# Performance work log

Measured on AMD Instinct MI355X. Metric: run time of the kernel, lower is better.

Reference implementation:

```python
import jax, jax.numpy as jnp
import numpy as np
from jax import lax

WS = 8            # window size
N = WS * WS       # tokens per window = 64
HEADS = 4
QKV_DIM = 16      # per-head dim
INNER = HEADS * QKV_DIM  # 64
SCALE = 1.0 / float(np.sqrt(QKV_DIM))


def setup_inputs() -> dict:
    key = jax.random.key(0)
    ks = jax.random.split(key, 8)
    B, C, H, W = 8, 96, 192, 192
    O = 96
    p = lambda k, shape, s=0.02: jax.random.normal(k, shape, dtype=jnp.float32) * s
    return {
        "x": jax.random.normal(ks[0], (B, C, H, W), dtype=jnp.float32),
        "bias": p(ks[1], (1, N)),                   # learned per-window bias seed
        "bias_proj_w": p(ks[2], (N * N, N)),        # Linear(N, N*N, bias=False)
        "qkv_w": p(ks[3], (3 * INNER, C)),
        "qkv_b": jnp.zeros((3 * INNER,), jnp.float32),
        "out_w": p(ks[4], (C, INNER)),
        "out_b": jnp.zeros((C,), jnp.float32),
        "conv1_w": p(ks[5], (O, C, 1, 1)),
        "conv1_b": jnp.zeros((O,), jnp.float32),
        "conv2_w": p(ks[6], (O, O, 3, 3)),
        "conv2_b": jnp.zeros((O,), jnp.float32),
    }


def _leaky(x):
    return jnp.where(x >= 0, x, 0.1 * x)


def reference(x, bias, bias_proj_w, qkv_w, qkv_b, out_w, out_b,
              conv1_w, conv1_b, conv2_w, conv2_b):
    B, C, H, W = x.shape
    nh, nw = H // WS, W // WS

    # learned attention bias: Linear(N -> N*N) on (1,N) seed, viewed as (N,N)
    attn_bias = (bias @ bias_proj_w.T).reshape(N, N)

    # --- Window MHA (norm1 = Identity) ---
    # window partition: (B, C, H, W) -> (B*nh*nw, N, C)
    xw = x.reshape(B, C, nh, WS, nw, WS).transpose(0, 2, 4, 3, 5, 1)
    xw = xw.reshape(B * nh * nw, N, C)

    qkv = xw @ qkv_w.T + qkv_b                     # (Bw, N, 3*INNER)
    qkv = qkv.reshape(-1, N, 3, HEADS, QKV_DIM)
    q = qkv[:, :, 0].transpose(0, 2, 1, 3)         # (Bw, H, N, d)
    k = qkv[:, :, 1].transpose(0, 2, 1, 3)
    v = qkv[:, :, 2].transpose(0, 2, 1, 3)

    scores = jnp.einsum('bhnd,bhmd->bhnm', q, k) * SCALE + attn_bias
    attn = jax.nn.softmax(scores, axis=-1)
    o = jnp.einsum('bhnm,bhmd->bhnd', attn, v)     # (Bw, H, N, d)
    o = o.transpose(0, 2, 1, 3).reshape(-1, N, INNER)
    o = o @ out_w.T + out_b                        # (Bw, N, C)

    # window merge: (B*nh*nw, N, C) -> (B, C, H, W)
    o = o.reshape(B, nh, nw, WS, WS, C).transpose(0, 5, 1, 3, 2, 4)
    o = o.reshape(B, C, H, W)

    x = x + o                                      # residual

    # --- conv MLP: 1x1 conv -> LeakyReLU(0.1) -> 3x3 conv (replicate pad) -> LeakyReLU(0.1) ---
    h = jnp.einsum('oc,bchw->bohw', conv1_w[:, :, 0, 0], x) + conv1_b[None, :, None, None]
    h = _leaky(h)
    hp = jnp.pad(h, ((0, 0), (0, 0), (1, 1), (1, 1)), mode='edge')
    h = lax.conv_general_dilated(hp, conv2_w, (1, 1), 'VALID',
                                 dimension_numbers=('NCHW', 'OIHW', 'NCHW'))
    h = _leaky(h + conv2_b[None, :, None, None])

    # in_channels == out_channels -> proj is Identity
    return x + h
```

## Files before the change

### kernel.cpp

```cpp
#include <hip/hip_runtime.h>
#include <hip/hip_bf16.h>

typedef __attribute__((ext_vector_type(8))) short short8;
typedef __attribute__((ext_vector_type(4))) short short4v;
typedef __attribute__((ext_vector_type(4))) float floatx4;

#define MFMA16x32(a,b,c) __builtin_amdgcn_mfma_f32_16x16x32_bf16((a),(b),(c),0,0,0)

static __device__ __forceinline__ unsigned short f2b(float f) {
  __hip_bfloat16 h = __float2bfloat16(f);
  return __builtin_bit_cast(unsigned short, h);
}
static __device__ __forceinline__ float b2f(unsigned short u) {
  __hip_bfloat16 h = __builtin_bit_cast(__hip_bfloat16, u);
  return __bfloat162float(h);
}

#define HH 192
#define WWID 192
#define HW (192*192)

#define YX_OFF   0
#define H1_OFF   56623104
#define AB_OFF   113246208
#define QKVW_OFF 113262592
#define OUTW_OFF 113299456
#define W1_OFF   113311744
#define W2R_OFF  113330176

__global__ __launch_bounds__(256) void k_prep(
    const float* __restrict__ bias, const float* __restrict__ bpw,
    const float* __restrict__ qkv_w, const float* __restrict__ out_w,
    const float* __restrict__ w1, const float* __restrict__ w2,
    char* __restrict__ ws) {
  int tid = blockIdx.x * blockDim.x + threadIdx.x;
  int nth = gridDim.x * blockDim.x;
  float* ab = (float*)(ws + AB_OFF);
  unsigned short* qkvw = (unsigned short*)(ws + QKVW_OFF);
  unsigned short* outw = (unsigned short*)(ws + OUTW_OFF);
  unsigned short* w1b  = (unsigned short*)(ws + W1_OFF);
  unsigned short* w2r  = (unsigned short*)(ws + W2R_OFF);

  for (int i = tid; i < 4096; i += nth) {
    float s = 0.f;
    #pragma unroll 8
    for (int k = 0; k < 64; k++) s += bias[k] * bpw[i*64 + k];
    int c = i & 63;
    ab[(i & ~63) + ((c & 15) << 2) + (c >> 4)] = s;
  }
  for (int i = tid; i < 192*96; i += nth) qkvw[i] = f2b(qkv_w[i]);
  for (int i = tid; i < 96*64;  i += nth) outw[i] = f2b(out_w[i]);
  for (int i = tid; i < 96*96;  i += nth) w1b[i]  = f2b(w1[i]);
  for (int i = tid; i < 96*864; i += nth) {
    int o = i / 864, k = i % 864;
    int tap = k / 96, c = k % 96;
    w2r[i] = f2b(w2[(o*96 + c)*9 + tap]);
  }
}

__global__ __launch_bounds__(256) void k_xt(
    const float* __restrict__ x, unsigned short* __restrict__ xt) {
  __shared__ __align__(16) float tile[96*65];
  int blk = blockIdx.x;
  int b = blk / 576, rem = blk % 576;
  int i = rem / 3, j0 = (rem % 3) * 64;
  int tid = threadIdx.x;
  const float* xb = x + (size_t)b*96*HW + (size_t)i*WWID + j0;

  for (int f = tid; f < 1536; f += 256) {
    int c = f >> 4, q = f & 15;
    *(floatx4*)&tile[c*65 + 4*q] = *(const floatx4*)&xb[(size_t)c*HW + 4*q];
  }
  __syncthreads();
  unsigned short* xtb = xt + ((size_t)b*HW + (size_t)i*WWID + j0) * 96;
  for (int f = tid; f < 768; f += 256) {
    int p = f / 12, c0 = (f % 12) * 8;
    short8 o;
    #pragma unroll
    for (int u = 0; u < 8; u++) o[u] = (short)f2b(tile[(c0+u)*65 + p]);
    *(short8*)&xtb[p*96 + c0] = o;
  }
}

__global__ __launch_bounds__(256,4) void k_attn(
    unsigned short* yx, const float* __restrict__ qkv_b,
    const float* __restrict__ out_b, const float* __restrict__ b1,
    const char* __restrict__ wsr, unsigned short* __restrict__ h1) {
  __shared__ __align__(16) char smem[33792];
  unsigned short* vt   = (unsigned short*)smem;
  unsigned short* qkw  = (unsigned short*)(smem + 9216);
  unsigned short* o64  = (unsigned short*)smem;
  unsigned short* ybuf = (unsigned short*)(smem + 9216);

  const float* ab = (const float*)(wsr + AB_OFF);
  const unsigned short* qkvw = (const unsigned short*)(wsr + QKVW_OFF);
  const unsigned short* outw = (const unsigned short*)(wsr + OUTW_OFF);
  const unsigned short* w1b  = (const unsigned short*)(wsr + W1_OFF);

  int blk = blockIdx.x;
  int b = blk / 576, rem = blk % 576;
  int wi = rem / 24, wj = rem % 24;
  int h0 = wi * 8, w0 = wj * 8;
  unsigned short* xtw = yx + (size_t)b*HW*96;
  unsigned short* h1w = h1 + (size_t)b*HW*96;

  int tid = threadIdx.x;
  int h = tid >> 6, ln = tid & 63;
  int row = ln & 15, kg = ln >> 4;

  unsigned short* qh = qkw + h*3072;
  unsigned short* kh = qh + 1536;
  unsigned short* pch = qh;

  const floatx4 zf = {0.f, 0.f, 0.f, 0.f};
  const short8 zs = {0,0,0,0,0,0,0,0};

  floatx4 accq[4][3];
  #pragma unroll
  for (int m = 0; m < 4; m++)
    #pragma unroll
    for (int n = 0; n < 3; n++) accq[m][n] = zf;
  #pragma unroll
  for (int ks = 0; ks < 3; ks++) {
    int c0 = ks*32 + kg*8;
    short8 a[4], bb[3];
    #pragma unroll
    for (int m = 0; m < 4; m++) {
      int t = m*16 + row;
      a[m] = *(const short8*)&xtw[((size_t)((h0 + (t>>3))*WWID + w0 + (t&7)))*96 + c0];
    }
    #pragma unroll
    for (int n = 0; n < 3; n++)
      bb[n] = *(const short8*)&qkvw[((n*4 + h)*16 + row)*96 + c0];
    #pragma unroll
    for (int m = 0; m < 4; m++)
      #pragma unroll
      for (int n = 0; n < 3; n++) accq[m][n] = MFMA16x32(a[m], bb[n], accq[m][n]);
  }
  float qb0 = qkv_b[h*16 + row], qb1 = qkv_b[64 + h*16 + row], qb2 = qkv_b[128 + h*16 + row];
  #pragma unroll
  for (int m = 0; m < 4; m++) {
    #pragma unroll
    for (int r = 0; r < 4; r++) {
      int t = m*16 + kg*4 + r;
      qh[t*24 + row] = f2b(accq[m][0][r] + qb0);
      kh[t*24 + row] = f2b(accq[m][1][r] + qb1);
    }
    short4v vv;
    #pragma unroll
    for (int r = 0; r < 4; r++) vv[r] = (short)f2b(accq[m][2][r] + qb2);
    *(short4v*)&vt[(h*16 + row)*72 + m*16 + kg*4] = vv;
  }
  asm volatile("" ::: "memory");

  short8 kb[4];
  #pragma unroll
  for (int n = 0; n < 4; n++)
    kb[n] = (kg < 2) ? *(const short8*)&kh[(n*16 + row)*24 + kg*8] : zs;
  unsigned pw[4][4][2];
  float inv[4][4];
  #pragma unroll
  for (int m = 0; m < 4; m++) {
    short8 qa = (kg < 2) ? *(const short8*)&qh[(m*16 + row)*24 + kg*8] : zs;
    floatx4 sc[4];
    #pragma unroll
    for (int n = 0; n < 4; n++) sc[n] = MFMA16x32(qa, kb[n], zf);
    #pragma unroll
    for (int r = 0; r < 4; r++) {
      int t = m*16 + kg*4 + r;
      floatx4 abv = *(const floatx4*)&ab[t*64 + row*4];
      float e0 = __expf(sc[0][r]*0.25f + abv[0]);
      float e1 = __expf(sc[1][r]*0.25f + abv[1]);
      float e2 = __expf(sc[2][r]*0.25f + abv[2]);
      float e3 = __expf(sc[3][r]*0.25f + abv[3]);
      float s = (e0 + e1) + (e2 + e3);
      #pragma unroll
      for (int d = 1; d < 16; d <<= 1) s += __shfl_xor(s, d, 64);
      inv[m][r] = 1.0f / s;
      pw[m][r][0] = (unsigned)f2b(e0) | ((unsigned)f2b(e1) << 16);
      pw[m][r][1] = (unsigned)f2b(e2) | ((unsigned)f2b(e3) << 16);
    }
  }

  floatx4 ov[4];
  #pragma unroll
  for (int m = 0; m < 4; m++) ov[m] = zf;
  #pragma unroll
  for (int ksk = 0; ksk < 2; ksk++) {
    asm volatile("" ::: "memory");
    #pragma unroll
    for (int m = 0; m < 4; m++)
      #pragma unroll
      for (int r = 0; r < 4; r++) {
        int t = m*16 + kg*4 + r;
        unsigned w = pw[m][r][ksk];
        pch[t*40 + row]      = (unsigned short)w;
        pch[t*40 + 16 + row] = (unsigned short)(w >> 16);
      }
    asm volatile("" ::: "memory");
    short8 vb = *(const short8*)&vt[(h*16 + row)*72 + ksk*32 + kg*8];
    #pragma unroll
    for (int m = 0; m < 4; m++) {
      short8 pa = *(const short8*)&pch[(m*16 + row)*40 + kg*8];
      ov[m] = MFMA16x32(pa, vb, ov[m]);
    }
  }
  __syncthreads();

  #pragma unroll
  for (int m = 0; m < 4; m++)
    #pragma unroll
    for (int r = 0; r < 4; r++)
      o64[(m*16 + kg*4 + r)*72 + h*16 + row] = f2b(ov[m][r] * inv[m][r]);
  __syncthreads();

  floatx4 op[6];
  #pragma unroll
  for (int n = 0; n < 6; n++) op[n] = zf;
  #pragma unroll
  for (int ks = 0; ks < 2; ks++) {
    short8 ao = *(const short8*)&o64[(h*16 + row)*72 + ks*32 + kg*8];
    #pragma unroll
    for (int n = 0; n < 6; n++) {
      short8 bo = *(const short8*)&outw[(n*16 + row)*64 + ks*32 + kg*8];
      op[n] = MFMA16x32(ao, bo, op[n]);
    }
  }

  #pragma unroll
  for (int n = 0; n < 6; n++) {
    int o = n*16 + row;
    float ob = out_b[o];
    #pragma unroll
    for (int r = 0; r < 4; r++) {
      int t = h*16 + kg*4 + r;
      int gi = h0 + (t>>3), gj = w0 + (t&7);
      size_t gx = ((size_t)(gi*WWID + gj))*96 + o;
      float yv = op[n][r] + ob + b2f(xtw[gx]);
      unsigned short yb = f2b(yv);
      xtw[gx] = yb;
      ybuf[t*104 + o] = yb;
    }
  }
  asm volatile("" ::: "memory");

  floatx4 ac1[6];
  #pragma unroll
  for (int n = 0; n < 6; n++) ac1[n] = zf;
  #pragma unroll
  for (int ks = 0; ks < 3; ks++) {
    int c0 = ks*32 + kg*8;
    short8 ay = *(const short8*)&ybuf[(h*16 + row)*104 + c0];
    #pragma unroll
    for (int n = 0; n < 6; n++) {
      short8 bw = *(const short8*)&w1b[(n*16 + row)*96 + c0];
      ac1[n] = MFMA16x32(ay, bw, ac1[n]);
    }
  }
  #pragma unroll
  for (int n = 0; n < 6; n++) {
    int o = n*16 + row;
    float bo = b1[o];
    #pragma unroll
    for (int r = 0; r < 4; r++) {
      int t = h*16 + kg*4 + r;
      int gi = h0 + (t>>3), gj = w0 + (t&7);
      float v = ac1[n][r] + bo;
      v = v >= 0.f ? v : 0.1f*v;
      h1w[((size_t)(gi*WWID + gj))*96 + o] = f2b(v);
    }
  }
}

#define C2_CS 2760

__global__ __launch_bounds__(512,4) void k_conv2(
    const unsigned short* __restrict__ h1, const unsigned short* __restrict__ y,
    const float* __restrict__ b2, const char* __restrict__ wsr,
    float* __restrict__ out) {
  __shared__ __align__(16) char smem[66304];
  unsigned short* h1t = (unsigned short*)smem;
  float* ost = (float*)smem;
  const unsigned short* w2r = (const unsigned short*)(wsr + W2R_OFF);
  int blk = blockIdx.x;
  int b = blk / 144, rem = blk % 144;
  int i0 = (rem / 6) * 8, j0 = (rem % 6) * 32;
  int tid = threadIdx.x;

  for (int idx = tid; idx < 4080; idx += 512) {
    int pix = idx / 12, c8 = idx % 12;
    int hr = pix / 34, hc = pix % 34;
    int gi = min(max(i0 + hr - 1, 0), 191);
    int gj = min(max(j0 + hc - 1, 0), 191);
    *(short8*)&h1t[c8*C2_CS + pix*8] =
        *(const short8*)&h1[((size_t)b*HW + (size_t)gi*WWID + gj)*96 + c8*8];
  }
  __syncthreads();

  int wv = tid >> 6, ln = tid & 63;
  int row = ln & 15, kg = ln >> 4;
  int og = wv >> 2, pg = wv & 3;

  const floatx4 zf = {0.f, 0.f, 0.f, 0.f};
  floatx4 acc[3][4];
  #pragma unroll
  for (int m = 0; m < 3; m++)
    #pragma unroll
    for (int n = 0; n < 4; n++) acc[m][n] = zf;

  #pragma unroll
  for (int s = 0; s < 27; s++) {
    int tap = s / 3, di = tap / 3, dj = tap % 3;
    int cq = (s % 3)*4 + kg;
    short8 a[3], bb[4];
    #pragma unroll
    for (int m = 0; m < 3; m++)
      a[m] = *(const short8*)&w2r[(og*48 + m*16 + row)*864 + s*32 + kg*8];
    #pragma unroll
    for (int n = 0; n < 4; n++) {
      int p = pg*64 + n*16 + row;
      int pr = p >> 5, pc = p & 31;
      int pix = (pr + di)*34 + pc + dj;
      bb[n] = *(const short8*)&h1t[cq*C2_CS + pix*8];
    }
    #pragma unroll
    for (int m = 0; m < 3; m++)
      #pragma unroll
      for (int n = 0; n < 4; n++)
        acc[m][n] = MFMA16x32(a[m], bb[n], acc[m][n]);
  }
  __syncthreads();

  #pragma unroll
  for (int pass = 0; pass < 2; pass++) {
    if (og == pass) {
      #pragma unroll
      for (int m = 0; m < 3; m++) {
        #pragma unroll
        for (int r = 0; r < 4; r++) {
          int o2 = m*16 + kg*4 + r;
          int o = og*48 + o2;
          float bo = b2[o];
          #pragma unroll
          for (int n = 0; n < 4; n++) {
            int p = pg*64 + n*16 + row;
            int pr = p >> 5, pc = p & 31;
            float hv = acc[m][n][r] + bo;
            hv = hv >= 0.f ? hv : 0.1f*hv;
            float yv = b2f(y[((size_t)b*HW + (size_t)(i0+pr)*WWID + j0+pc)*96 + o]);
            ost[o2*260 + pr*32 + pc] = yv + hv;
          }
        }
      }
    }
    __syncthreads();
    for (int c = tid; c < 3072; c += 512) {
      int o2 = c >> 6, rq = c & 63;
      int pr = rq >> 3, q = rq & 7;
      floatx4 v = *(const floatx4*)&ost[o2*260 + pr*32 + q*4];
      int o = pass*48 + o2;
      *(floatx4*)&out[((size_t)(b*96 + o)*HH + i0 + pr)*WWID + j0 + q*4] = v;
    }
    __syncthreads();
  }
}

extern "C" void kernel_launch(void* const* d_in, const int* in_sizes, int n_in,
                              void* d_out, int out_size, void* d_ws, size_t ws_size,
                              hipStream_t stream) {
  const float* x    = (const float*)d_in[0];
  const float* bias = (const float*)d_in[1];
  const float* bpw  = (const float*)d_in[2];
  const float* qkvw = (const float*)d_in[3];
  const float* qkvb = (const float*)d_in[4];
  const float* outw = (const float*)d_in[5];
  const float* outb = (const float*)d_in[6];
  const float* w1   = (const float*)d_in[7];
  const float* b1   = (const float*)d_in[8];
  const float* w2   = (const float*)d_in[9];
  const float* b2   = (const float*)d_in[10];

  char* ws = (char*)d_ws;
  float* out = (float*)d_out;
  unsigned short* yx = (unsigned short*)(ws + YX_OFF);
  unsigned short* h1 = (unsigned short*)(ws + H1_OFF);

  k_prep<<<128, 256, 0, stream>>>(bias, bpw, qkvw, outw, w1, w2, ws);
  k_xt  <<<4608, 256, 0, stream>>>(x, yx);
  k_attn<<<4608, 256, 0, stream>>>(yx, qkvb, outb, b1, ws, h1);
  k_conv2<<<1152, 512, 0, stream>>>(h1, yx, b2, ws, out);
}
```

Measured before the change: 267.0 us.

## Switch conv2 LDS tile to pixel-major padded layout and store output directly

Changes the conv2 shared-memory tile from a channel-group-major layout to a pixel-major layout with 104-element padded rows. It also removes the LDS-staged two-pass epilogue, writing results straight to global memory from the accumulators, and drops the full unroll of the 27-step tap loop. This is meant to cut LDS footprint and barriers and to change bank-conflict behaviour on the B-operand reads. In exchange, the output stores become strided scalar writes instead of coalesced float4 rows.

```diff
diff --git a/kernel.cpp b/kernel.cpp
--- a/kernel.cpp
+++ b/kernel.cpp
@@ -272,15 +272,11 @@
   }
 }
 
-#define C2_CS 2760
-
 __global__ __launch_bounds__(512,4) void k_conv2(
     const unsigned short* __restrict__ h1, const unsigned short* __restrict__ y,
     const float* __restrict__ b2, const char* __restrict__ wsr,
     float* __restrict__ out) {
-  __shared__ __align__(16) char smem[66304];
-  unsigned short* h1t = (unsigned short*)smem;
-  float* ost = (float*)smem;
+  __shared__ __align__(16) unsigned short h1t[340*104];
   const unsigned short* w2r = (const unsigned short*)(wsr + W2R_OFF);
   int blk = blockIdx.x;
   int b = blk / 144, rem = blk % 144;
@@ -288,12 +284,12 @@
   int tid = threadIdx.x;
 
   for (int idx = tid; idx < 4080; idx += 512) {
-    int pix = idx / 12, c8 = idx % 12;
+    int pix = idx / 12, cc = (idx % 12) * 8;
     int hr = pix / 34, hc = pix % 34;
     int gi = min(max(i0 + hr - 1, 0), 191);
     int gj = min(max(j0 + hc - 1, 0), 191);
-    *(short8*)&h1t[c8*C2_CS + pix*8] =
-        *(const short8*)&h1[((size_t)b*HW + (size_t)gi*WWID + gj)*96 + c8*8];
+    *(short8*)&h1t[pix*104 + cc] =
+        *(const short8*)&h1[((size_t)b*HW + (size_t)gi*WWID + gj)*96 + cc];
   }
   __syncthreads();
 
@@ -308,10 +304,9 @@
     #pragma unroll
     for (int n = 0; n < 4; n++) acc[m][n] = zf;
 
-  #pragma unroll
   for (int s = 0; s < 27; s++) {
-    int tap = s / 3, di = tap / 3, dj = tap % 3;
-    int cq = (s % 3)*4 + kg;
+    int tap = s / 3, c0 = (s % 3) * 32;
+    int di = tap / 3, dj = tap % 3;
     short8 a[3], bb[4];
     #pragma unroll
     for (int m = 0; m < 3; m++)
@@ -320,8 +315,7 @@
     for (int n = 0; n < 4; n++) {
       int p = pg*64 + n*16 + row;
       int pr = p >> 5, pc = p & 31;
-      int pix = (pr + di)*34 + pc + dj;
-      bb[n] = *(const short8*)&h1t[cq*C2_CS + pix*8];
+      bb[n] = *(const short8*)&h1t[((pr + di)*34 + pc + dj)*104 + c0 + kg*8];
     }
     #pragma unroll
     for (int m = 0; m < 3; m++)
@@ -329,39 +323,23 @@
       for (int n = 0; n < 4; n++)
         acc[m][n] = MFMA16x32(a[m], bb[n], acc[m][n]);
   }
-  __syncthreads();
-
-  #pragma unroll
-  for (int pass = 0; pass < 2; pass++) {
-    if (og == pass) {
-      #pragma unroll
-      for (int m = 0; m < 3; m++) {
-        #pragma unroll
-        for (int r = 0; r < 4; r++) {
-          int o2 = m*16 + kg*4 + r;
-          int o = og*48 + o2;
-          float bo = b2[o];
-          #pragma unroll
-          for (int n = 0; n < 4; n++) {
-            int p = pg*64 + n*16 + row;
-            int pr = p >> 5, pc = p & 31;
-            float hv = acc[m][n][r] + bo;
-            hv = hv >= 0.f ? hv : 0.1f*hv;
-            float yv = b2f(y[((size_t)b*HW + (size_t)(i0+pr)*WWID + j0+pc)*96 + o]);
-            ost[o2*260 + pr*32 + pc] = yv + hv;
-          }
-        }
+
+  #pragma unroll
+  for (int m = 0; m < 3; m++) {
+    #pragma unroll
+    for (int r = 0; r < 4; r++) {
+      int o = og*48 + m*16 + kg*4 + r;
+      float bo = b2[o];
+      #pragma unroll
+      for (int n = 0; n < 4; n++) {
+        int p = pg*64 + n*16 + row;
+        int pr = p >> 5, pc = p & 31;
+        float hv = acc[m][n][r] + bo;
+        hv = hv >= 0.f ? hv : 0.1f*hv;
+        float yv = b2f(y[((size_t)b*HW + (size_t)(i0+pr)*WWID + j0+pc)*96 + o]);
+        out[((size_t)(b*96 + o)*HH + i0 + pr)*WWID + j0 + pc] = yv + hv;
       }
     }
-    __syncthreads();
-    for (int c = tid; c < 3072; c += 512) {
-      int o2 = c >> 6, rq = c & 63;
-      int pr = rq >> 3, q = rq & 7;
-      floatx4 v = *(const floatx4*)&ost[o2*260 + pr*32 + q*4];
-      int o = pass*48 + o2;
-      *(floatx4*)&out[((size_t)(b*96 + o)*HH + i0 + pr)*WWID + j0 + q*4] = v;
-    }
-    __syncthreads();
   }
 }
 
```

After: 240.0 us. 1.11x faster.
